# Kernel tuning notes

Hardware: AMD Instinct MI355X
Metric: run time of the kernel (lower is better)

The kernel has to match this reference:

```python
import jax, jax.numpy as jnp
import numpy as np

C = 1024   # hidden_size
H = 16     # num_heads
D = C // H # head dim
M = 4096   # mlp hidden
T = 1024   # motion seq len
B = 8      # batch
TA = 1024  # audio seq len


def _w(key, shape):
    return jax.random.normal(key, shape, dtype=jnp.float32) * 0.02


def setup_inputs() -> dict:
    key = jax.random.key(0)
    ks = jax.random.split(key, 32)
    inp = {
        'x': jax.random.normal(ks[0], (T, B, C), dtype=jnp.float32),
        'c': jax.random.normal(ks[1], (B, C), dtype=jnp.float32),
        'padding_mask': jax.random.randint(ks[2], (B, T), 0, 2, dtype=jnp.int32),
        'audio_seq': jax.random.normal(ks[3], (TA, B, C), dtype=jnp.float32),
        'audio_mask': jax.random.randint(ks[4], (B, TA), 0, 2, dtype=jnp.int32),
        # adaLN modulation: SiLU -> Linear(C, 6C)
        'w_ada': _w(ks[5], (C, 6 * C)), 'b_ada': jnp.zeros((6 * C,), jnp.float32),
        # self-attention q/k/v/proj
        'wq': _w(ks[6], (C, C)), 'bq': jnp.zeros((C,), jnp.float32),
        'wk': _w(ks[7], (C, C)), 'bk': jnp.zeros((C,), jnp.float32),
        'wv': _w(ks[8], (C, C)), 'bv': jnp.zeros((C,), jnp.float32),
        'wo': _w(ks[9], (C, C)), 'bo': jnp.zeros((C,), jnp.float32),
        # cross-attention q/k/v/proj
        'cwq': _w(ks[10], (C, C)), 'cbq': jnp.zeros((C,), jnp.float32),
        'cwk': _w(ks[11], (C, C)), 'cbk': jnp.zeros((C,), jnp.float32),
        'cwv': _w(ks[12], (C, C)), 'cbv': jnp.zeros((C,), jnp.float32),
        'cwo': _w(ks[13], (C, C)), 'cbo': jnp.zeros((C,), jnp.float32),
        # MLP fc1/fc2
        'w1': _w(ks[14], (C, M)), 'b1': jnp.zeros((M,), jnp.float32),
        'w2': _w(ks[15], (M, C)), 'b2': jnp.zeros((C,), jnp.float32),
    }
    return inp


def _ln(x):
    # LayerNorm(elementwise_affine=False, eps=1e-6)
    mu = jnp.mean(x, axis=-1, keepdims=True)
    var = jnp.var(x, axis=-1, keepdims=True)
    return (x - mu) * jax.lax.rsqrt(var + 1e-6)


def _modulate(x, shift, scale):
    # batch-first x [B, T, C]; shift/scale [B, C]
    return x * (1.0 + scale[:, None, :]) + shift[:, None, :]


def _mha(xq, xkv, wq, bq, wk, bk, wv, bv, wo, bo, mask):
    # xq [B, Tq, C], xkv [B, Tk, C], mask [B, Tk] (nonzero = masked)
    b, tq, _ = xq.shape
    tk = xkv.shape[1]
    q = (xq @ wq + bq).reshape(b, tq, H, D)
    k = (xkv @ wk + bk).reshape(b, tk, H, D)
    v = (xkv @ wv + bv).reshape(b, tk, H, D)
    att = jnp.einsum('bqhd,bkhd->bhqk', q, k) * (1.0 / np.sqrt(D))
    att = jnp.where(mask[:, None, None, :] != 0, -jnp.inf, att)
    att = jax.nn.softmax(att, axis=-1)
    y = jnp.einsum('bhqk,bkhd->bqhd', att, v).reshape(b, tq, C)
    return y @ wo + bo


def _gelu_tanh(x):
    return jax.nn.gelu(x, approximate=True)


def reference(x, c, padding_mask, audio_seq, audio_mask,
              w_ada, b_ada, wq, bq, wk, bk, wv, bv, wo, bo,
              cwq, cbq, cwk, cbk, cwv, cbv, cwo, cbo,
              w1, b1, w2, b2):
    # adaLN modulation parameters
    mod = jax.nn.silu(c) @ w_ada + b_ada                 # [B, 6C]
    (shift_msa, scale_msa, gate_msa,
     shift_mlp, scale_mlp, gate_mlp) = jnp.split(mod, 6, axis=1)

    # x is sequence-first [T, B, C] (padding_mask batch dim matches x dim 1)
    x_batch = jnp.transpose(x, (1, 0, 2))                # [B, T, C]
    x_mod = _modulate(_ln(x_batch), shift_msa, scale_msa)
    attn_out = _mha(x_mod, x_mod, wq, bq, wk, bk, wv, bv, wo, bo, padding_mask)
    x = x + gate_msa[None, :, :] * jnp.transpose(attn_out, (1, 0, 2))

    # cross attention (reuses msa shift/scale/gate, as in the source)
    xb = jnp.transpose(x, (1, 0, 2))                     # [B, T, C]
    ab = jnp.transpose(audio_seq, (1, 0, 2))             # [B, TA, C]
    x_cross_in = _modulate(_ln(xb), shift_msa, scale_msa)
    cross_out = _mha(x_cross_in, ab, cwq, cbq, cwk, cbk, cwv, cbv, cwo, cbo,
                     audio_mask)
    x = x + gate_msa[None, :, :] * jnp.transpose(cross_out, (1, 0, 2))

    # MLP
    xb = jnp.transpose(x, (1, 0, 2))
    h = _modulate(_ln(xb), shift_mlp, scale_mlp)
    mlp_out = _gelu_tanh(h @ w1 + b1) @ w2 + b2
    x = x + gate_mlp[None, :, :] * jnp.transpose(mlp_out, (1, 0, 2))
    return x
```

## Files before the change

### kernel.cpp

```cpp
#include <hip/hip_runtime.h>
#include <math.h>

#define T_SEQ 1024
#define TA_SEQ 1024
#define BATCH 8
#define CH 1024
#define NH 16
#define HD 64
#define MH 4096

typedef unsigned short u16;
typedef unsigned short u16x4 __attribute__((ext_vector_type(4)));
typedef unsigned short u16x8 __attribute__((ext_vector_type(8)));
typedef __bf16 bf16x8 __attribute__((ext_vector_type(8)));
typedef float f32x4 __attribute__((ext_vector_type(4)));

__device__ __forceinline__ u16 f2bf(float f) {
  unsigned int u = __builtin_bit_cast(unsigned int, f);
  u += 0x7FFFu + ((u >> 16) & 1u);
  return (u16)(u >> 16);
}
__device__ __forceinline__ u16 f2bf_trunc(float f) {
  return (u16)(__builtin_bit_cast(unsigned int, f) >> 16);
}
__device__ __forceinline__ bf16x8 ldbf8(const u16* p) {
  return __builtin_bit_cast(bf16x8, *reinterpret_cast<const u16x8*>(p));
}
__device__ __forceinline__ void gload_lds16(const u16* g, u16* l) {
  __builtin_amdgcn_global_load_lds(
      (const __attribute__((address_space(1))) unsigned int*)g,
      (__attribute__((address_space(3))) unsigned int*)l, 16, 0, 0);
}

#define ASM_BAR()   asm volatile("s_barrier" ::: "memory")
#define ASM_VM4()   asm volatile("s_waitcnt vmcnt(4)" ::: "memory")
#define ASM_VM0()   asm volatile("s_waitcnt vmcnt(0)" ::: "memory")
#define ASM_LGKM0() asm volatile("s_waitcnt lgkmcnt(0)" ::: "memory")

__global__ void k_transpose_w(const float* __restrict__ in, u16* __restrict__ out,
                              int K, int N) {
  __shared__ float tile[32][33];
  int n0 = blockIdx.x * 32, k0 = blockIdx.y * 32;
  int tx = threadIdx.x, ty = threadIdx.y;
#pragma unroll
  for (int i = 0; i < 4; i++)
    tile[ty + i * 8][tx] = in[(size_t)(k0 + ty + i * 8) * N + n0 + tx];
  __syncthreads();
#pragma unroll
  for (int i = 0; i < 4; i++)
    out[(size_t)(n0 + ty + i * 8) * K + k0 + tx] = f2bf(tile[tx][ty + i * 8]);
}

struct P8f { const float* p[8]; };
struct P8u { u16* p[8]; };
__global__ void k_transpose8(P8f in8, P8u out8) {
  const float* __restrict__ in = in8.p[blockIdx.z];
  u16* __restrict__ out = out8.p[blockIdx.z];
  __shared__ float tile[32][33];
  int n0 = blockIdx.x * 32, k0 = blockIdx.y * 32;
  int tx = threadIdx.x, ty = threadIdx.y;
#pragma unroll
  for (int i = 0; i < 4; i++)
    tile[ty + i * 8][tx] = in[(size_t)(k0 + ty + i * 8) * CH + n0 + tx];
  __syncthreads();
#pragma unroll
  for (int i = 0; i < 4; i++)
    out[(size_t)(n0 + ty + i * 8) * CH + k0 + tx] = f2bf(tile[tx][ty + i * 8]);
}

__global__ void k_ada(const float* __restrict__ c, const float* __restrict__ w_ada,
                      const float* __restrict__ b_ada, float* __restrict__ mod) {
  __shared__ float sc[CH];
  int b = blockIdx.y;
  int tid = threadIdx.x;
  for (int i = tid; i < CH; i += 256) {
    float cv = c[b * CH + i];
    sc[i] = cv / (1.0f + expf(-cv));
  }
  __syncthreads();
  int n = blockIdx.x * 256 + tid;
  float acc = 0.0f;
  for (int k = 0; k < CH; k++) acc += sc[k] * w_ada[(size_t)k * (6 * CH) + n];
  mod[(size_t)b * (6 * CH) + n] = acc + b_ada[n];
}

__global__ void k_tbc_to_btc_f32(const float* __restrict__ in, float* __restrict__ out) {
  size_t i = (size_t)blockIdx.x * 256 + threadIdx.x;
  int c = (int)(i & (CH - 1));
  size_t tb = i >> 10;
  int b = (int)(tb & (BATCH - 1));
  size_t t = tb >> 3;
  out[((size_t)b * T_SEQ + t) * CH + c] = in[i];
}
__global__ void k_tbc_to_btc_bf16(const float* __restrict__ in, u16* __restrict__ out) {
  size_t i = (size_t)blockIdx.x * 256 + threadIdx.x;
  int c = (int)(i & (CH - 1));
  size_t tb = i >> 10;
  int b = (int)(tb & (BATCH - 1));
  size_t t = tb >> 3;
  out[((size_t)b * TA_SEQ + t) * CH + c] = f2bf(in[i]);
}

__global__ void k_ln_mod(const float* __restrict__ xb, const float* __restrict__ mod,
                         u16* __restrict__ out, int shift_sel, int scale_sel) {
  int row = blockIdx.x;
  int b = row >> 10;
  int tid = threadIdx.x;
  const float* xr = xb + (size_t)row * CH;
  float4 v = reinterpret_cast<const float4*>(xr)[tid];
  float s = v.x + v.y + v.z + v.w;
  float s2 = v.x * v.x + v.y * v.y + v.z * v.z + v.w * v.w;
#pragma unroll
  for (int off = 32; off > 0; off >>= 1) {
    s += __shfl_down(s, off);
    s2 += __shfl_down(s2, off);
  }
  __shared__ float red[8];
  __shared__ float stats[2];
  int wid = tid >> 6;
  if ((tid & 63) == 0) { red[wid] = s; red[4 + wid] = s2; }
  __syncthreads();
  if (tid == 0) {
    float a = red[0] + red[1] + red[2] + red[3];
    float a2 = red[4] + red[5] + red[6] + red[7];
    float mu = a * (1.0f / CH);
    float var = a2 * (1.0f / CH) - mu * mu;
    stats[0] = mu;
    stats[1] = rsqrtf(var + 1e-6f);
  }
  __syncthreads();
  float mu = stats[0], rs = stats[1];
  int c0 = tid * 4;
  const float* sh = mod + (size_t)b * (6 * CH) + (size_t)shift_sel * CH + c0;
  const float* scl = mod + (size_t)b * (6 * CH) + (size_t)scale_sel * CH + c0;
  float xs[4] = {v.x, v.y, v.z, v.w};
  u16x4 o;
#pragma unroll
  for (int j = 0; j < 4; j++)
    o[j] = f2bf((xs[j] - mu) * rs * (1.0f + scl[j]) + sh[j]);
  *reinterpret_cast<u16x4*>(out + (size_t)row * CH + c0) = o;
}

__device__ __forceinline__ void gemm_compute(const u16* As, const u16* Bs,
                                             int wm, int wn, int lrow, int sx,
                                             f32x4 (&acc)[4][4]) {
  bf16x8 af[4], bfr[4];
#pragma unroll
  for (int mi = 0; mi < 4; mi++)
    af[mi] = ldbf8(&As[(wm + mi * 16 + lrow) * 32 + sx]);
#pragma unroll
  for (int ni = 0; ni < 4; ni++)
    bfr[ni] = ldbf8(&Bs[(wn + ni * 16 + lrow) * 32 + sx]);
#pragma unroll
  for (int mi = 0; mi < 4; mi++)
#pragma unroll
    for (int ni = 0; ni < 4; ni++)
      acc[mi][ni] = __builtin_amdgcn_mfma_f32_16x16x32_bf16(af[mi], bfr[ni],
                                                            acc[mi][ni], 0, 0, 0);
}

__device__ __forceinline__ void gemm_core(
    const u16* __restrict__ A, const u16* __restrict__ Bt, int K,
    int m0, int n0, int tid, u16* As, u16* Bs, f32x4 (&acc)[4][4]) {
  int wid = tid >> 6, lane = tid & 63;
  int wm = (wid >> 1) * 64, wn = (wid & 1) * 64;
  int lrow = lane & 15, quad = lane >> 4;
  int sx = (quad ^ ((lrow >> 1) & 3)) * 8;
  int c0 = tid, c1 = 256 + tid;
  int r0 = c0 >> 2, r1 = c1 >> 2;
  int q0 = ((c0 & 3) ^ ((r0 >> 1) & 3)) * 8;
  int q1 = ((c1 & 3) ^ ((r1 >> 1) & 3)) * 8;
  const u16* ga0 = A + (size_t)(m0 + r0) * K + q0;
  const u16* ga1 = A + (size_t)(m0 + r1) * K + q1;
  const u16* gb0 = Bt + (size_t)(n0 + r0) * K + q0;
  const u16* gb1 = Bt + (size_t)(n0 + r1) * K + q1;
  u16* la0 = As + c0 * 8;
  u16* la1 = As + c1 * 8;
  u16* lb0 = Bs + c0 * 8;
  u16* lb1 = Bs + c1 * 8;
  auto stage = [&](int tile, int boff) {
    int ko = tile << 5;
    gload_lds16(ga0 + ko, la0 + boff);
    gload_lds16(ga1 + ko, la1 + boff);
    gload_lds16(gb0 + ko, lb0 + boff);
    gload_lds16(gb1 + ko, lb1 + boff);
  };
  const int kiters = K >> 5;
  stage(0, 0);
  stage(1, 4096);
  int kt = 0;
  for (; kt + 4 < kiters; kt += 3) {
    ASM_LGKM0(); ASM_VM4(); ASM_BAR();
    stage(kt + 2, 8192);
    gemm_compute(As, Bs, wm, wn, lrow, sx, acc);
    ASM_LGKM0(); ASM_VM4(); ASM_BAR();
    stage(kt + 3, 0);
    gemm_compute(As + 4096, Bs + 4096, wm, wn, lrow, sx, acc);
    ASM_LGKM0(); ASM_VM4(); ASM_BAR();
    stage(kt + 4, 4096);
    gemm_compute(As + 8192, Bs + 8192, wm, wn, lrow, sx, acc);
  }
  ASM_LGKM0(); ASM_VM4(); ASM_BAR();
  gemm_compute(As, Bs, wm, wn, lrow, sx, acc);
  ASM_LGKM0(); ASM_VM0(); ASM_BAR();
  gemm_compute(As + 4096, Bs + 4096, wm, wn, lrow, sx, acc);
}

template <int EPI>
__global__ __launch_bounds__(256) void k_gemm(
    const u16* __restrict__ A, const u16* __restrict__ Bt,
    const float* __restrict__ bias, u16* __restrict__ out_bf,
    float* __restrict__ xb, const float* __restrict__ mod, int gate_sel,
    int M, int N, int K) {
  __shared__ u16 As[3 * 128 * 32];
  __shared__ u16 Bs[3 * 128 * 32];
  int m0 = blockIdx.x * 128, n0 = blockIdx.y * 128;
  int tid = threadIdx.x;
  int wid = tid >> 6, lane = tid & 63;
  int wm = (wid >> 1) * 64, wn = (wid & 1) * 64;
  int lrow = lane & 15, quad = lane >> 4;
  f32x4 acc[4][4];
#pragma unroll
  for (int mi = 0; mi < 4; mi++)
#pragma unroll
    for (int ni = 0; ni < 4; ni++) acc[mi][ni] = {0.f, 0.f, 0.f, 0.f};
  gemm_core(A, Bt, K, m0, n0, tid, As, Bs, acc);
#pragma unroll
  for (int mi = 0; mi < 4; mi++)
#pragma unroll
    for (int ni = 0; ni < 4; ni++) {
      int col = n0 + wn + ni * 16 + lrow;
      float bval = bias[col];
#pragma unroll
      for (int r = 0; r < 4; r++) {
        int row = m0 + wm + mi * 16 + quad * 4 + r;
        float v = acc[mi][ni][r] + bval;
        if (EPI == 1) {
          int b = row >> 10;
          float g = mod[(size_t)b * (6 * CH) + (size_t)gate_sel * CH + col];
          xb[(size_t)row * N + col] += g * v;
        } else if (EPI == 2) {
          float t2 = 2.3021181302f * (v + 0.044715f * v * v * v);
          float gel = v * __builtin_amdgcn_rcpf(1.0f + exp2f(-t2));
          out_bf[(size_t)row * N + col] = f2bf(gel);
        } else {
          out_bf[(size_t)row * N + col] = f2bf(v * 0.18033688011112042f);
        }
      }
    }
}

__global__ __launch_bounds__(256) void k_gemm_qkv(
    const u16* __restrict__ A, const u16* __restrict__ Bt,
    const float* __restrict__ bq, const float* __restrict__ bk,
    const float* __restrict__ bv,
    u16* __restrict__ qout, u16* __restrict__ kout, u16* __restrict__ vt) {
  __shared__ u16 As[3 * 128 * 32];
  __shared__ u16 Bs[3 * 128 * 32];
  int m0 = blockIdx.x * 128, n0 = blockIdx.y * 128;
  int tid = threadIdx.x;
  int wid = tid >> 6, lane = tid & 63;
  int wm = (wid >> 1) * 64, wn = (wid & 1) * 64;
  int lrow = lane & 15, quad = lane >> 4;
  f32x4 acc[4][4];
#pragma unroll
  for (int mi = 0; mi < 4; mi++)
#pragma unroll
    for (int ni = 0; ni < 4; ni++) acc[mi][ni] = {0.f, 0.f, 0.f, 0.f};
  gemm_core(A, Bt, CH, m0, n0, tid, As, Bs, acc);
  int seg = n0 >> 10;
  const float* bias = (seg == 0) ? bq : (seg == 1) ? bk : bv;
#pragma unroll
  for (int mi = 0; mi < 4; mi++)
#pragma unroll
    for (int ni = 0; ni < 4; ni++) {
      int col = (n0 & 1023) + wn + ni * 16 + lrow;
      float bval = bias[col];
      int row0 = m0 + wm + mi * 16 + quad * 4;
      if (seg == 0) {
#pragma unroll
        for (int r = 0; r < 4; r++)
          qout[(size_t)(row0 + r) * CH + col] =
              f2bf((acc[mi][ni][r] + bval) * 0.18033688011112042f);
      } else if (seg == 1) {
#pragma unroll
        for (int r = 0; r < 4; r++)
          kout[(size_t)(row0 + r) * CH + col] = f2bf(acc[mi][ni][r] + bval);
      } else {
        u16x4 pk;
#pragma unroll
        for (int r = 0; r < 4; r++) pk[r] = f2bf(acc[mi][ni][r] + bval);
        int b = row0 >> 10, t0 = row0 & 1023;
        int h = col >> 6, d = col & 63;
        *reinterpret_cast<u16x4*>(
            vt + (((size_t)(b * NH + h) * HD + d) << 10) + t0) = pk;
      }
    }
}

__global__ __launch_bounds__(256) void k_gemm_kv(
    const u16* __restrict__ A, const u16* __restrict__ Bt,
    const float* __restrict__ bk, const float* __restrict__ bv,
    u16* __restrict__ kout, u16* __restrict__ vt) {
  __shared__ u16 As[3 * 128 * 32];
  __shared__ u16 Bs[3 * 128 * 32];
  int m0 = blockIdx.x * 128, n0 = blockIdx.y * 128;
  int tid = threadIdx.x;
  int wid = tid >> 6, lane = tid & 63;
  int wm = (wid >> 1) * 64, wn = (wid & 1) * 64;
  int lrow = lane & 15, quad = lane >> 4;
  f32x4 acc[4][4];
#pragma unroll
  for (int mi = 0; mi < 4; mi++)
#pragma unroll
    for (int ni = 0; ni < 4; ni++) acc[mi][ni] = {0.f, 0.f, 0.f, 0.f};
  gemm_core(A, Bt, CH, m0, n0, tid, As, Bs, acc);
  int seg = n0 >> 10;
  const float* bias = (seg == 0) ? bk : bv;
#pragma unroll
  for (int mi = 0; mi < 4; mi++)
#pragma unroll
    for (int ni = 0; ni < 4; ni++) {
      int col = (n0 & 1023) + wn + ni * 16 + lrow;
      float bval = bias[col];
      int row0 = m0 + wm + mi * 16 + quad * 4;
      if (seg == 0) {
#pragma unroll
        for (int r = 0; r < 4; r++)
          kout[(size_t)(row0 + r) * CH + col] = f2bf(acc[mi][ni][r] + bval);
      } else {
        u16x4 pk;
#pragma unroll
        for (int r = 0; r < 4; r++) pk[r] = f2bf(acc[mi][ni][r] + bval);
        int b = row0 >> 10, t0 = row0 & 1023;
        int h = col >> 6, d = col & 63;
        *reinterpret_cast<u16x4*>(
            vt + (((size_t)(b * NH + h) * HD + d) << 10) + t0) = pk;
      }
    }
}

__global__ __launch_bounds__(256, 2) void k_attn(
    const u16* __restrict__ Q, const u16* __restrict__ Kb,
    const u16* __restrict__ vt, const int* __restrict__ mask,
    u16* __restrict__ Y) {
  int qt = blockIdx.x, h = blockIdx.y, b = blockIdx.z;
  int tid = threadIdx.x, wid = tid >> 6, lane = tid & 63;
  int lrow = lane & 15, quad = lane >> 4;
  int qbase = qt * 256 + wid * 64;

  __shared__ u16 P[4][4][16][72];

  bf16x8 aq[4][2];
#pragma unroll
  for (int st = 0; st < 4; st++) {
    size_t qoff = ((size_t)(b * T_SEQ + qbase + st * 16 + lrow)) * CH + h * HD;
    aq[st][0] = ldbf8(Q + qoff + quad * 8);
    aq[st][1] = ldbf8(Q + qoff + 32 + quad * 8);
  }

  u16x8 uo;
#pragma unroll
  for (int j = 0; j < 8; j++) uo[j] = (lrow == 0) ? (u16)0x3F80 : (u16)0;
  bf16x8 ones = __builtin_bit_cast(bf16x8, uo);

  const int* mrow = mask + (size_t)b * T_SEQ;
  const u16* ksrc = Kb + ((size_t)(b * T_SEQ) + lrow) * CH + h * HD + quad * 8;
  const u16* vsrc = vt + (((size_t)(b * NH + h) * HD + lrow) << 10) + quad * 8;

  f32x4 o[4][5];
#pragma unroll
  for (int st = 0; st < 4; st++)
#pragma unroll
    for (int dc = 0; dc < 5; dc++) o[st][dc] = {0.f, 0.f, 0.f, 0.f};

  for (int kt = 0; kt < 16; kt++) {
    int kb = kt * 64;
    bf16x8 kf[8];
    float mb[4];
#pragma unroll
    for (int sub = 0; sub < 4; sub++) {
      const u16* kp = ksrc + (size_t)(kb + sub * 16) * CH;
      kf[sub * 2] = ldbf8(kp);
      kf[sub * 2 + 1] = ldbf8(kp + 32);
      mb[sub] = mrow[kb + sub * 16 + lrow] ? -INFINITY : 0.0f;
    }
    bf16x8 vf[8];
#pragma unroll
    for (int dc = 0; dc < 4; dc++) {
      const u16* vp = vsrc + (size_t)(dc * 16) * 1024 + kb;
      vf[dc * 2] = ldbf8(vp);
      vf[dc * 2 + 1] = ldbf8(vp + 32);
    }
#pragma unroll
    for (int st = 0; st < 4; st++) {
#pragma unroll
      for (int sub = 0; sub < 4; sub++) {
        f32x4 z = {0.f, 0.f, 0.f, 0.f};
        z = __builtin_amdgcn_mfma_f32_16x16x32_bf16(aq[st][0], kf[sub * 2], z, 0, 0, 0);
        z = __builtin_amdgcn_mfma_f32_16x16x32_bf16(aq[st][1], kf[sub * 2 + 1], z, 0, 0, 0);
        float mbv = mb[sub];
#pragma unroll
        for (int r = 0; r < 4; r++) {
          float p = exp2f(z[r] + mbv);
          P[wid][st][quad * 4 + r][sub * 16 + lrow] = f2bf_trunc(p);
        }
      }
    }
#pragma unroll
    for (int st = 0; st < 4; st++) {
      bf16x8 pf0 = ldbf8(&P[wid][st][lrow][quad * 8]);
      bf16x8 pf1 = ldbf8(&P[wid][st][lrow][32 + quad * 8]);
#pragma unroll
      for (int dc = 0; dc < 4; dc++) {
        o[st][dc] = __builtin_amdgcn_mfma_f32_16x16x32_bf16(pf0, vf[dc * 2], o[st][dc], 0, 0, 0);
        o[st][dc] = __builtin_amdgcn_mfma_f32_16x16x32_bf16(pf1, vf[dc * 2 + 1], o[st][dc], 0, 0, 0);
      }
      o[st][4] = __builtin_amdgcn_mfma_f32_16x16x32_bf16(pf0, ones, o[st][4], 0, 0, 0);
      o[st][4] = __builtin_amdgcn_mfma_f32_16x16x32_bf16(pf1, ones, o[st][4], 0, 0, 0);
    }
  }

#pragma unroll
  for (int st = 0; st < 4; st++)
#pragma unroll
    for (int r = 0; r < 4; r++) {
      float l = __shfl(o[st][4][r], lane & 48);
      float linv = 1.0f / l;
      int qr = qbase + st * 16 + quad * 4 + r;
      size_t yo = ((size_t)(b * T_SEQ + qr)) * CH + h * HD;
#pragma unroll
      for (int dc = 0; dc < 4; dc++)
        Y[yo + dc * 16 + lrow] = f2bf(o[st][dc][r] * linv);
    }
}

__global__ void k_out(const float* __restrict__ xb, float* __restrict__ out) {
  size_t i = (size_t)blockIdx.x * 256 + threadIdx.x;
  int c = (int)(i & (CH - 1));
  size_t tb = i >> 10;
  int b = (int)(tb & (BATCH - 1));
  size_t t = tb >> 3;
  out[i] = xb[((size_t)b * T_SEQ + t) * CH + c];
}

extern "C" void kernel_launch(void* const* d_in, const int* in_sizes, int n_in,
                              void* d_out, int out_size, void* d_ws, size_t ws_size,
                              hipStream_t stream) {
  const float* x     = (const float*)d_in[0];
  const float* c     = (const float*)d_in[1];
  const int*   pmask = (const int*)d_in[2];
  const float* audio = (const float*)d_in[3];
  const int*   amask = (const int*)d_in[4];
  const float* w_ada = (const float*)d_in[5];
  const float* b_ada = (const float*)d_in[6];
  const float* wq = (const float*)d_in[7];  const float* bq = (const float*)d_in[8];
  const float* wk = (const float*)d_in[9];  const float* bk = (const float*)d_in[10];
  const float* wv = (const float*)d_in[11]; const float* bv = (const float*)d_in[12];
  const float* wo = (const float*)d_in[13]; const float* bo = (const float*)d_in[14];
  const float* cwq = (const float*)d_in[15]; const float* cbq = (const float*)d_in[16];
  const float* cwk = (const float*)d_in[17]; const float* cbk = (const float*)d_in[18];
  const float* cwv = (const float*)d_in[19]; const float* cbv = (const float*)d_in[20];
  const float* cwo = (const float*)d_in[21]; const float* cbo = (const float*)d_in[22];
  const float* w1 = (const float*)d_in[23]; const float* b1 = (const float*)d_in[24];
  const float* w2 = (const float*)d_in[25]; const float* b2 = (const float*)d_in[26];

  char* wsb = (char*)d_ws;
  size_t off = 0;
  auto alloc = [&](size_t bytes) {
    char* p = wsb + off;
    off += (bytes + 255) & ~(size_t)255;
    return p;
  };
  const size_t SQ = (size_t)CH * CH * 2;
  u16* wqT  = (u16*)alloc(SQ);
  u16* wkT  = (u16*)alloc(SQ);
  u16* wvT  = (u16*)alloc(SQ);
  u16* woT  = (u16*)alloc(SQ);
  u16* cwqT = (u16*)alloc(SQ);
  u16* cwkT = (u16*)alloc(SQ);
  u16* cwvT = (u16*)alloc(SQ);
  u16* cwoT = (u16*)alloc(SQ);
  u16* w1T  = (u16*)alloc((size_t)CH * MH * 2);
  u16* w2T  = (u16*)alloc((size_t)CH * MH * 2);
  float* mod = (float*)alloc((size_t)BATCH * 6 * CH * 4);
  float* xb  = (float*)alloc((size_t)BATCH * T_SEQ * CH * 4);
  u16* xm    = (u16*)alloc((size_t)BATCH * T_SEQ * CH * 2);
  u16* hbuf  = (u16*)alloc((size_t)BATCH * T_SEQ * MH * 2);
  u16* qbuf  = hbuf;
  u16* kbuf  = hbuf + (size_t)BATCH * T_SEQ * CH;
  u16* ybuf  = hbuf + (size_t)2 * BATCH * T_SEQ * CH;
  u16* vt    = hbuf + (size_t)3 * BATCH * T_SEQ * CH;
  u16* abuf  = (u16*)alloc((size_t)BATCH * TA_SEQ * CH * 2);
  (void)ws_size; (void)in_sizes; (void)n_in; (void)out_size;

  const int NE = T_SEQ * BATCH * CH;
  dim3 tb32(32, 8);

  P8f src8; P8u dst8;
  src8.p[0] = wq;  dst8.p[0] = wqT;
  src8.p[1] = wk;  dst8.p[1] = wkT;
  src8.p[2] = wv;  dst8.p[2] = wvT;
  src8.p[3] = wo;  dst8.p[3] = woT;
  src8.p[4] = cwq; dst8.p[4] = cwqT;
  src8.p[5] = cwk; dst8.p[5] = cwkT;
  src8.p[6] = cwv; dst8.p[6] = cwvT;
  src8.p[7] = cwo; dst8.p[7] = cwoT;
  k_transpose8<<<dim3(CH / 32, CH / 32, 8), tb32, 0, stream>>>(src8, dst8);
  k_transpose_w<<<dim3(MH / 32, CH / 32), tb32, 0, stream>>>(w1, w1T, CH, MH);
  k_transpose_w<<<dim3(CH / 32, MH / 32), tb32, 0, stream>>>(w2, w2T, MH, CH);

  k_ada<<<dim3(6 * CH / 256, BATCH), 256, 0, stream>>>(c, w_ada, b_ada, mod);
  k_tbc_to_btc_f32<<<NE / 256, 256, 0, stream>>>(x, xb);
  k_tbc_to_btc_bf16<<<NE / 256, 256, 0, stream>>>(audio, abuf);

  k_ln_mod<<<BATCH * T_SEQ, 256, 0, stream>>>(xb, mod, xm, 0, 1);
  k_gemm_qkv<<<dim3(64, 24), 256, 0, stream>>>(xm, wqT, bq, bk, bv, qbuf, kbuf, vt);
  k_attn<<<dim3(T_SEQ / 256, NH, BATCH), 256, 0, stream>>>(qbuf, kbuf, vt, pmask, ybuf);
  k_gemm<1><<<dim3(64, 8), 256, 0, stream>>>(ybuf, woT, bo, nullptr, xb, mod, 2, 8192, CH, CH);

  k_ln_mod<<<BATCH * T_SEQ, 256, 0, stream>>>(xb, mod, xm, 0, 1);
  k_gemm<3><<<dim3(64, 8), 256, 0, stream>>>(xm, cwqT, cbq, qbuf, nullptr, nullptr, 0, 8192, CH, CH);
  k_gemm_kv<<<dim3(64, 16), 256, 0, stream>>>(abuf, cwkT, cbk, cbv, kbuf, vt);
  k_attn<<<dim3(T_SEQ / 256, NH, BATCH), 256, 0, stream>>>(qbuf, kbuf, vt, amask, ybuf);
  k_gemm<1><<<dim3(64, 8), 256, 0, stream>>>(ybuf, cwoT, cbo, nullptr, xb, mod, 2, 8192, CH, CH);

  k_ln_mod<<<BATCH * T_SEQ, 256, 0, stream>>>(xb, mod, xm, 3, 4);
  k_gemm<2><<<dim3(64, 32), 256, 0, stream>>>(xm, w1T, b1, hbuf, nullptr, nullptr, 0, 8192, MH, CH);
  k_gemm<1><<<dim3(64, 8), 256, 0, stream>>>(hbuf, w2T, b2, nullptr, xb, mod, 5, 8192, CH, MH);

  k_out<<<NE / 256, 256, 0, stream>>>(xb, (float*)d_out);
}
```

Measured before the change: 927.3 us.

## Add 256x256-tile 8-wave GEMM core for QKV, cross-KV and MLP fc1

Introduces a new GEMM core using 256x256 output tiles with 512 threads (8 waves, each computing 128x64), a K-step of 64 split into two 32-wide halves, double-buffered direct-to-LDS loads with swizzling, and interleaved load/MFMA phases with setprio. The QKV, cross-attention KV and fc1 GEMMs switch to this core, cutting global/LDS traffic per FLOP through larger tile reuse. In exchange, register pressure rises (32 accumulators per wave), LDS use is 128KB per block, and grids shrink to 384/256/512 blocks, which may underfill the 256 CUs or leave tail imbalance.

```diff
diff --git a/kernel.cpp b/kernel.cpp
--- a/kernel.cpp
+++ b/kernel.cpp
@@ -33,6 +33,7 @@
 }
 
 #define ASM_BAR()   asm volatile("s_barrier" ::: "memory")
+#define ASM_VM8()   asm volatile("s_waitcnt vmcnt(8)" ::: "memory")
 #define ASM_VM4()   asm volatile("s_waitcnt vmcnt(4)" ::: "memory")
 #define ASM_VM0()   asm volatile("s_waitcnt vmcnt(0)" ::: "memory")
 #define ASM_LGKM0() asm volatile("s_waitcnt lgkmcnt(0)" ::: "memory")
@@ -250,33 +251,155 @@
     }
 }
 
-__global__ __launch_bounds__(256) void k_gemm_qkv(
+__device__ __forceinline__ void mfma_quad(const bf16x8 (&af)[4], const bf16x8 (&bfr)[4],
+                                          f32x4 (*arow)[4]) {
+#pragma unroll
+  for (int mi = 0; mi < 4; mi++)
+#pragma unroll
+    for (int ni = 0; ni < 4; ni++)
+      arow[mi][ni] = __builtin_amdgcn_mfma_f32_16x16x32_bf16(af[mi], bfr[ni],
+                                                             arow[mi][ni], 0, 0, 0);
+}
+
+__device__ __forceinline__ void gemm256_core(
+    const u16* __restrict__ A, const u16* __restrict__ Bt, int K,
+    int m0, int n0, int tid, u16* AS, u16* BS, f32x4 (&acc)[8][4]) {
+  int wid = tid >> 6, lane = tid & 63;
+  int wr = wid >> 2, wc = wid & 3;
+  int lrow = lane & 15, quad = lane >> 4;
+  int sx = (quad ^ ((lrow >> 1) & 3)) * 8;
+  int aRow = wr * 128 + lrow;
+  int bRow = wc * 64 + lrow;
+  int rA = tid >> 2;
+  int qsw = (((tid & 3) ^ ((tid >> 3) & 3)) << 3);
+  const u16* gA = A + (size_t)(m0 + rA) * K + qsw;
+  const u16* gB = Bt + (size_t)(n0 + rA) * K + qsw;
+  const size_t r128 = (size_t)128 * K;
+  u16* dA = AS + tid * 8;
+  u16* dB = BS + tid * 8;
+  const int NT = K >> 6;
+
+#define STGA(dd, hh, tt) do { const u16* s_ = gA + ((tt) * 64 + (hh) * 32); \
+    u16* d_ = dA + ((dd) * 2 + (hh)) * 8192; \
+    gload_lds16(s_, d_); gload_lds16(s_ + r128, d_ + 4096); } while (0)
+#define STGB(dd, hh, tt) do { const u16* s_ = gB + ((tt) * 64 + (hh) * 32); \
+    u16* d_ = dB + ((dd) * 2 + (hh)) * 8192; \
+    gload_lds16(s_, d_); gload_lds16(s_ + r128, d_ + 4096); } while (0)
+#define RD_A(dd, kk, mh) do { const u16* b_ = AS + ((dd) * 2 + (kk)) * 8192; \
+    int r_ = aRow + (mh) * 64; \
+    af[0] = ldbf8(&b_[(r_) * 32 + sx]); \
+    af[1] = ldbf8(&b_[(r_ + 16) * 32 + sx]); \
+    af[2] = ldbf8(&b_[(r_ + 32) * 32 + sx]); \
+    af[3] = ldbf8(&b_[(r_ + 48) * 32 + sx]); } while (0)
+#define RD_B(dd, kk) do { const u16* b_ = BS + ((dd) * 2 + (kk)) * 8192; \
+    bfr[0] = ldbf8(&b_[(bRow) * 32 + sx]); \
+    bfr[1] = ldbf8(&b_[(bRow + 16) * 32 + sx]); \
+    bfr[2] = ldbf8(&b_[(bRow + 32) * 32 + sx]); \
+    bfr[3] = ldbf8(&b_[(bRow + 48) * 32 + sx]); } while (0)
+#define PHASE_TAIL(mh) do { ASM_LGKM0(); __builtin_amdgcn_sched_barrier(0); \
+    __builtin_amdgcn_s_setprio(1); mfma_quad(af, bfr, acc + (mh) * 4); \
+    __builtin_amdgcn_s_setprio(0); ASM_BAR(); } while (0)
+
+  STGA(0, 0, 0); STGB(0, 0, 0); STGA(0, 1, 0); STGB(0, 1, 0);
+  STGA(1, 0, 1); STGB(1, 0, 1);
+  ASM_VM8(); ASM_BAR();
+
+  bf16x8 af[4], bfr[4];
+  for (int t = 0; t < NT; ++t) {
+    int d = t & 1;
+    RD_A(d, 0, 0); RD_B(d, 0);
+    if (t + 1 < NT) STGA(d ^ 1, 1, t + 1);
+    PHASE_TAIL(0);
+    RD_A(d, 0, 1);
+    if (t + 1 < NT) STGB(d ^ 1, 1, t + 1);
+    if (t == NT - 1) { ASM_VM0(); } else { ASM_VM8(); }
+    PHASE_TAIL(1);
+    RD_A(d, 1, 0); RD_B(d, 1);
+    if (t + 2 < NT) STGA(d, 0, t + 2);
+    PHASE_TAIL(0);
+    RD_A(d, 1, 1);
+    if (t + 2 < NT) STGB(d, 0, t + 2);
+    if (t < NT - 2) { ASM_VM8(); } else if (t == NT - 2) { ASM_VM4(); }
+    PHASE_TAIL(1);
+  }
+#undef STGA
+#undef STGB
+#undef RD_A
+#undef RD_B
+#undef PHASE_TAIL
+}
+
+template <int EPI>
+__global__ __launch_bounds__(512, 2) void k_gemm256(
+    const u16* __restrict__ A, const u16* __restrict__ Bt,
+    const float* __restrict__ bias, u16* __restrict__ out_bf,
+    float* __restrict__ xb, const float* __restrict__ mod, int gate_sel,
+    int M, int N, int K) {
+  __shared__ u16 AS[2 * 2 * 8192];
+  __shared__ u16 BS[2 * 2 * 8192];
+  int m0 = blockIdx.x * 256, n0 = blockIdx.y * 256;
+  int tid = threadIdx.x;
+  int wid = tid >> 6, lane = tid & 63;
+  int wr = wid >> 2, wc = wid & 3;
+  int lrow = lane & 15, quad = lane >> 4;
+  f32x4 acc[8][4];
+#pragma unroll
+  for (int mi = 0; mi < 8; mi++)
+#pragma unroll
+    for (int ni = 0; ni < 4; ni++) acc[mi][ni] = {0.f, 0.f, 0.f, 0.f};
+  gemm256_core(A, Bt, K, m0, n0, tid, AS, BS, acc);
+#pragma unroll
+  for (int mi = 0; mi < 8; mi++)
+#pragma unroll
+    for (int ni = 0; ni < 4; ni++) {
+      int col = n0 + wc * 64 + ni * 16 + lrow;
+      float bval = bias[col];
+#pragma unroll
+      for (int r = 0; r < 4; r++) {
+        int row = m0 + wr * 128 + mi * 16 + quad * 4 + r;
+        float v = acc[mi][ni][r] + bval;
+        if (EPI == 1) {
+          int b = row >> 10;
+          float g = mod[(size_t)b * (6 * CH) + (size_t)gate_sel * CH + col];
+          xb[(size_t)row * N + col] += g * v;
+        } else if (EPI == 2) {
+          float t2 = 2.3021181302f * (v + 0.044715f * v * v * v);
+          float gel = v * __builtin_amdgcn_rcpf(1.0f + exp2f(-t2));
+          out_bf[(size_t)row * N + col] = f2bf(gel);
+        } else {
+          out_bf[(size_t)row * N + col] = f2bf(v * 0.18033688011112042f);
+        }
+      }
+    }
+}
+
+__global__ __launch_bounds__(512, 2) void k_qkv256(
     const u16* __restrict__ A, const u16* __restrict__ Bt,
     const float* __restrict__ bq, const float* __restrict__ bk,
     const float* __restrict__ bv,
     u16* __restrict__ qout, u16* __restrict__ kout, u16* __restrict__ vt) {
-  __shared__ u16 As[3 * 128 * 32];
-  __shared__ u16 Bs[3 * 128 * 32];
-  int m0 = blockIdx.x * 128, n0 = blockIdx.y * 128;
+  __shared__ u16 AS[2 * 2 * 8192];
+  __shared__ u16 BS[2 * 2 * 8192];
+  int m0 = blockIdx.x * 256, n0 = blockIdx.y * 256;
   int tid = threadIdx.x;
   int wid = tid >> 6, lane = tid & 63;
-  int wm = (wid >> 1) * 64, wn = (wid & 1) * 64;
+  int wr = wid >> 2, wc = wid & 3;
   int lrow = lane & 15, quad = lane >> 4;
-  f32x4 acc[4][4];
-#pragma unroll
-  for (int mi = 0; mi < 4; mi++)
+  f32x4 acc[8][4];
+#pragma unroll
+  for (int mi = 0; mi < 8; mi++)
 #pragma unroll
     for (int ni = 0; ni < 4; ni++) acc[mi][ni] = {0.f, 0.f, 0.f, 0.f};
-  gemm_core(A, Bt, CH, m0, n0, tid, As, Bs, acc);
+  gemm256_core(A, Bt, CH, m0, n0, tid, AS, BS, acc);
   int seg = n0 >> 10;
   const float* bias = (seg == 0) ? bq : (seg == 1) ? bk : bv;
 #pragma unroll
-  for (int mi = 0; mi < 4; mi++)
+  for (int mi = 0; mi < 8; mi++)
 #pragma unroll
     for (int ni = 0; ni < 4; ni++) {
-      int col = (n0 & 1023) + wn + ni * 16 + lrow;
+      int col = (n0 & 1023) + wc * 64 + ni * 16 + lrow;
       float bval = bias[col];
-      int row0 = m0 + wm + mi * 16 + quad * 4;
+      int row0 = m0 + wr * 128 + mi * 16 + quad * 4;
       if (seg == 0) {
 #pragma unroll
         for (int r = 0; r < 4; r++)
@@ -298,32 +421,32 @@
     }
 }
 
-__global__ __launch_bounds__(256) void k_gemm_kv(
+__global__ __launch_bounds__(512, 2) void k_kv256(
     const u16* __restrict__ A, const u16* __restrict__ Bt,
     const float* __restrict__ bk, const float* __restrict__ bv,
     u16* __restrict__ kout, u16* __restrict__ vt) {
-  __shared__ u16 As[3 * 128 * 32];
-  __shared__ u16 Bs[3 * 128 * 32];
-  int m0 = blockIdx.x * 128, n0 = blockIdx.y * 128;
+  __shared__ u16 AS[2 * 2 * 8192];
+  __shared__ u16 BS[2 * 2 * 8192];
+  int m0 = blockIdx.x * 256, n0 = blockIdx.y * 256;
   int tid = threadIdx.x;
   int wid = tid >> 6, lane = tid & 63;
-  int wm = (wid >> 1) * 64, wn = (wid & 1) * 64;
+  int wr = wid >> 2, wc = wid & 3;
   int lrow = lane & 15, quad = lane >> 4;
-  f32x4 acc[4][4];
-#pragma unroll
-  for (int mi = 0; mi < 4; mi++)
+  f32x4 acc[8][4];
+#pragma unroll
+  for (int mi = 0; mi < 8; mi++)
 #pragma unroll
     for (int ni = 0; ni < 4; ni++) acc[mi][ni] = {0.f, 0.f, 0.f, 0.f};
-  gemm_core(A, Bt, CH, m0, n0, tid, As, Bs, acc);
+  gemm256_core(A, Bt, CH, m0, n0, tid, AS, BS, acc);
   int seg = n0 >> 10;
   const float* bias = (seg == 0) ? bk : bv;
 #pragma unroll
-  for (int mi = 0; mi < 4; mi++)
+  for (int mi = 0; mi < 8; mi++)
 #pragma unroll
     for (int ni = 0; ni < 4; ni++) {
-      int col = (n0 & 1023) + wn + ni * 16 + lrow;
+      int col = (n0 & 1023) + wc * 64 + ni * 16 + lrow;
       float bval = bias[col];
-      int row0 = m0 + wm + mi * 16 + quad * 4;
+      int row0 = m0 + wr * 128 + mi * 16 + quad * 4;
       if (seg == 0) {
 #pragma unroll
         for (int r = 0; r < 4; r++)
@@ -515,18 +638,18 @@
   k_tbc_to_btc_bf16<<<NE / 256, 256, 0, stream>>>(audio, abuf);
 
   k_ln_mod<<<BATCH * T_SEQ, 256, 0, stream>>>(xb, mod, xm, 0, 1);
-  k_gemm_qkv<<<dim3(64, 24), 256, 0, stream>>>(xm, wqT, bq, bk, bv, qbuf, kbuf, vt);
+  k_qkv256<<<dim3(32, 12), 512, 0, stream>>>(xm, wqT, bq, bk, bv, qbuf, kbuf, vt);
   k_attn<<<dim3(T_SEQ / 256, NH, BATCH), 256, 0, stream>>>(qbuf, kbuf, vt, pmask, ybuf);
   k_gemm<1><<<dim3(64, 8), 256, 0, stream>>>(ybuf, woT, bo, nullptr, xb, mod, 2, 8192, CH, CH);
 
   k_ln_mod<<<BATCH * T_SEQ, 256, 0, stream>>>(xb, mod, xm, 0, 1);
   k_gemm<3><<<dim3(64, 8), 256, 0, stream>>>(xm, cwqT, cbq, qbuf, nullptr, nullptr, 0, 8192, CH, CH);
-  k_gemm_kv<<<dim3(64, 16), 256, 0, stream>>>(abuf, cwkT, cbk, cbv, kbuf, vt);
+  k_kv256<<<dim3(32, 8), 512, 0, stream>>>(abuf, cwkT, cbk, cbv, kbuf, vt);
   k_attn<<<dim3(T_SEQ / 256, NH, BATCH), 256, 0, stream>>>(qbuf, kbuf, vt, amask, ybuf);
   k_gemm<1><<<dim3(64, 8), 256, 0, stream>>>(ybuf, cwoT, cbo, nullptr, xb, mod, 2, 8192, CH, CH);
 
   k_ln_mod<<<BATCH * T_SEQ, 256, 0, stream>>>(xb, mod, xm, 3, 4);
-  k_gemm<2><<<dim3(64, 32), 256, 0, stream>>>(xm, w1T, b1, hbuf, nullptr, nullptr, 0, 8192, MH, CH);
+  k_gemm256<2><<<dim3(32, 16), 512, 0, stream>>>(xm, w1T, b1, hbuf, nullptr, nullptr, 0, 8192, MH, CH);
   k_gemm<1><<<dim3(64, 8), 256, 0, stream>>>(hbuf, w2T, b2, nullptr, xb, mod, 5, 8192, CH, MH);
 
   k_out<<<NE / 256, 256, 0, stream>>>(xb, (float*)d_out);
```

Measured after the change: 892.8 us. 1.04x faster.
